# Optimization experiments

Measured on AMD Instinct MI355X. Metric: run time of the kernel, lower is better.

The kernel has to match this reference:

```python
import jax, jax.numpy as jnp
import numpy as np

V, T, H, N, HID = 512, 64, 256, 1024, 100
D = V + T  # biLSTM input dim


def _lstm_dir(x, Wih, Whh, b, reverse):
    # x: [n, Din]; PyTorch gate order i,f,g,o; b = b_ih + b_hh (equivalent math)
    xw = x @ Wih.T + b  # [n, 4H] precomputed input projection
    if reverse:
        xw = xw[::-1]
    h_dim = Whh.shape[1]

    def step(carry, xt):
        h, c = carry
        g = xt + h @ Whh.T
        i, f, gg, o = jnp.split(g, 4, axis=-1)
        i = jax.nn.sigmoid(i)
        f = jax.nn.sigmoid(f)
        gg = jnp.tanh(gg)
        o = jax.nn.sigmoid(o)
        c = f * c + i * gg
        h = o * jnp.tanh(c)
        return (h, c), h

    init = (jnp.zeros((h_dim,), x.dtype), jnp.zeros((h_dim,), x.dtype))
    _, hs = jax.lax.scan(step, init, xw)
    return hs[::-1] if reverse else hs


def setup_inputs() -> dict:
    key = jax.random.key(0)
    ks = jax.random.split(key, 20)
    s = 1.0 / np.sqrt(H)  # PyTorch LSTM init scale
    inp = {
        "word_table": jax.random.normal(ks[0], (V, V), jnp.float32) * 0.1,
        "pos_table": jax.random.normal(ks[1], (T, T), jnp.float32) * 0.1,
        # layer 0 fwd/bwd
        "l0f_Wih": jax.random.uniform(ks[2], (4 * H, D), jnp.float32, -s, s),
        "l0f_Whh": jax.random.uniform(ks[3], (4 * H, H), jnp.float32, -s, s),
        "l0f_b": jax.random.uniform(ks[4], (4 * H,), jnp.float32, -s, s),
        "l0b_Wih": jax.random.uniform(ks[5], (4 * H, D), jnp.float32, -s, s),
        "l0b_Whh": jax.random.uniform(ks[6], (4 * H, H), jnp.float32, -s, s),
        "l0b_b": jax.random.uniform(ks[7], (4 * H,), jnp.float32, -s, s),
        # layer 1 fwd/bwd (input = 2H)
        "l1f_Wih": jax.random.uniform(ks[8], (4 * H, 2 * H), jnp.float32, -s, s),
        "l1f_Whh": jax.random.uniform(ks[9], (4 * H, H), jnp.float32, -s, s),
        "l1f_b": jax.random.uniform(ks[10], (4 * H,), jnp.float32, -s, s),
        "l1b_Wih": jax.random.uniform(ks[11], (4 * H, 2 * H), jnp.float32, -s, s),
        "l1b_Whh": jax.random.uniform(ks[12], (4 * H, H), jnp.float32, -s, s),
        "l1b_b": jax.random.uniform(ks[13], (4 * H,), jnp.float32, -s, s),
        # edge-scorer MLP: Linear(4H,100) -> tanh -> Linear(100,1)
        "mlp_W1": jax.random.uniform(ks[14], (HID, 4 * H), jnp.float32, -0.03, 0.03),
        "mlp_b1": jax.random.uniform(ks[15], (HID,), jnp.float32, -0.03, 0.03),
        "mlp_W2": jax.random.uniform(ks[16], (1, HID), jnp.float32, -0.1, 0.1),
        "mlp_b2": jax.random.uniform(ks[17], (1,), jnp.float32, -0.1, 0.1),
        "word_idx": jax.random.randint(ks[18], (1, N), 0, V),
        "pos_idx": jax.random.randint(ks[19], (1, N), 0, T),
    }
    return inp


def reference(word_table, pos_table,
              l0f_Wih, l0f_Whh, l0f_b, l0b_Wih, l0b_Whh, l0b_b,
              l1f_Wih, l1f_Whh, l1f_b, l1b_Wih, l1b_Whh, l1b_b,
              mlp_W1, mlp_b1, mlp_W2, mlp_b2,
              word_idx, pos_idx):
    # embedding lookups on external tables, cat word+pos -> [n, D]
    x = jnp.concatenate([word_table[word_idx[0]], pos_table[pos_idx[0]]], axis=-1)
    # 2-layer bidirectional LSTM, batch=1 (squeezed)
    h = jnp.concatenate([_lstm_dir(x, l0f_Wih, l0f_Whh, l0f_b, False),
                         _lstm_dir(x, l0b_Wih, l0b_Whh, l0b_b, True)], axis=-1)  # [n, 2H]
    h = jnp.concatenate([_lstm_dir(h, l1f_Wih, l1f_Whh, l1f_b, False),
                         _lstm_dir(h, l1b_Wih, l1b_Whh, l1b_b, True)], axis=-1)  # [n, 2H]
    # pairwise edge scorer: layer_2(tanh(layer_1(cat(h_head, h_mod))))
    # split W1 = [Wh | Wm] so the cat never materializes per pair
    two_h = h.shape[-1]
    Wh, Wm = mlp_W1[:, :two_h], mlp_W1[:, two_h:]
    A = h @ Wh.T  # [n, HID] head contribution
    B = h @ Wm.T  # [n, HID] modifier contribution
    hid = jnp.tanh(A[:, None, :] + B[None, :, :] + mlp_b1)  # [n, n, HID]
    scores = hid @ mlp_W2[0] + mlp_b2[0]  # [n, n]
    n = scores.shape[0]
    eye = jnp.eye(n, dtype=bool)
    scores = jnp.where(eye, 0.0, scores)  # diagonal left at 0, as in the torch loop
    return jax.nn.softmax(scores, axis=0)
```

## Files before the change

kernel.cpp:

```cpp
#include <hip/hip_runtime.h>
#include <hip/hip_bf16.h>


#define L2E 1.4426950408889634f

__device__ __forceinline__ float fast_rcp(float x) { return __builtin_amdgcn_rcpf(x); }
__device__ __forceinline__ float sigm_f(float x) {
    return fast_rcp(1.f + exp2f(-x * L2E));
}
__device__ __forceinline__ float tanh_f(float x) {
    return 1.f - 2.f * fast_rcp(1.f + exp2f(x * (2.f * L2E)));
}

__device__ __forceinline__ void st_msg(unsigned long long* p, unsigned long long m) {
    asm volatile("global_store_dwordx2 %0, %1, off sc0 sc1"
                 :: "v"(p), "v"(m) : "memory");
}

__device__ __forceinline__ unsigned long long poll_msg(
    const unsigned long long* p, unsigned want)
{
    unsigned long long r0, r1, r2, r3, r = 0;
    bool done = false;
    for (int it = 0; it < 8192 && !done; ++it) {
        asm volatile(
            "global_load_dwordx2 %0, %4, off sc0 sc1\n\t"
            "global_load_dwordx2 %1, %4, off sc0 sc1\n\t"
            "global_load_dwordx2 %2, %4, off sc0 sc1\n\t"
            "global_load_dwordx2 %3, %4, off sc0 sc1\n\t"
            "s_waitcnt vmcnt(3)"
            : "=&v"(r0), "=&v"(r1), "=&v"(r2), "=&v"(r3)
            : "v"(p) : "memory");
        if (__all((unsigned)(r0 >> 32) == want)) { r = r0; done = true; }
        if (!done) {
            asm volatile("s_waitcnt vmcnt(2)" ::: "memory");
            if (__all((unsigned)(r1 >> 32) == want)) { r = r1; done = true; }
        }
        if (!done) {
            asm volatile("s_waitcnt vmcnt(1)" ::: "memory");
            if (__all((unsigned)(r2 >> 32) == want)) { r = r2; done = true; }
        }
        if (!done) {
            asm volatile("s_waitcnt vmcnt(0)" ::: "memory");
            if (__all((unsigned)(r3 >> 32) == want)) { r = r3; done = true; }
        }
        asm volatile("s_waitcnt vmcnt(0)" ::: "memory");
    }
    if (!done) {
        do {
            r = __hip_atomic_load(p, __ATOMIC_RELAXED, __HIP_MEMORY_SCOPE_AGENT);
        } while (!__all((unsigned)(r >> 32) == want));
    }
    return r;
}

__global__ __launch_bounds__(256) void embed_kernel(
    const float* __restrict__ wt, const float* __restrict__ pt,
    const int* __restrict__ wi, const int* __restrict__ pi,
    float* __restrict__ x)
{
    int idx = blockIdx.x * 256 + threadIdx.x;
    if (idx >= 1024 * 576) return;
    int n = idx / 576, c = idx % 576;
    x[idx] = (c < 512) ? wt[wi[n] * 512 + c] : pt[pi[n] * 64 + (c - 512)];
}

__global__ __launch_bounds__(256) void gemm_bias(
    const float* __restrict__ A,
    const float* __restrict__ W0, const float* __restrict__ W1,
    const float* __restrict__ b0, const float* __restrict__ b1,
    float* __restrict__ C0, float* __restrict__ C1,
    int M, int N, int K)
{
    const float* W = blockIdx.z ? W1 : W0;
    const float* bias = blockIdx.z ? b1 : b0;
    float* C = blockIdx.z ? C1 : C0;
    int m0 = blockIdx.y * 64, n0 = blockIdx.x * 64;
    __shared__ float As[16][65];
    __shared__ float Ws[16][65];
    int tid = threadIdx.x;
    int tx = tid & 15, ty = tid >> 4;
    float acc[4][4] = {};
    int lr = tid >> 2, lkc = (tid & 3) * 4;
    for (int k0 = 0; k0 < K; k0 += 16) {
        float4 a4 = *(const float4*)&A[(size_t)(m0 + lr) * K + k0 + lkc];
        float4 w4 = *(const float4*)&W[(size_t)(n0 + lr) * K + k0 + lkc];
        As[lkc + 0][lr] = a4.x; As[lkc + 1][lr] = a4.y;
        As[lkc + 2][lr] = a4.z; As[lkc + 3][lr] = a4.w;
        Ws[lkc + 0][lr] = w4.x; Ws[lkc + 1][lr] = w4.y;
        Ws[lkc + 2][lr] = w4.z; Ws[lkc + 3][lr] = w4.w;
        __syncthreads();
#pragma unroll
        for (int k = 0; k < 16; k++) {
            float a[4], b[4];
#pragma unroll
            for (int i = 0; i < 4; i++) a[i] = As[k][ty * 4 + i];
#pragma unroll
            for (int j = 0; j < 4; j++) b[j] = Ws[k][tx * 4 + j];
#pragma unroll
            for (int i = 0; i < 4; i++)
#pragma unroll
                for (int j = 0; j < 4; j++) acc[i][j] += a[i] * b[j];
        }
        __syncthreads();
    }
    int colbase = n0 + tx * 4;
    float4 bv = *(const float4*)&bias[colbase];
#pragma unroll
    for (int i = 0; i < 4; i++) {
        float4 o;
        o.x = acc[i][0] + bv.x; o.y = acc[i][1] + bv.y;
        o.z = acc[i][2] + bv.z; o.w = acc[i][3] + bv.w;
        *(float4*)&C[(size_t)(m0 + ty * 4 + i) * N + colbase] = o;
    }
}

__global__ __launch_bounds__(512, 2) void lstm_scan(
    const float* __restrict__ xw_f, const float* __restrict__ xw_b,
    const float* __restrict__ Whh_f, const float* __restrict__ Whh_b,
    float* __restrict__ hout,
    unsigned long long* __restrict__ hx)
{
    int slot = blockIdx.x & 7;
    int sub  = blockIdx.x >> 3;
    int dir;
    if (slot == 0) dir = 0;
    else if (slot == 4) dir = 1;
    else return;

    const float* __restrict__ xw  = dir ? xw_b : xw_f;
    const float* __restrict__ Whh = dir ? Whh_b : Whh_f;
    unsigned long long* __restrict__ hxd = hx + dir * 512;

    const int tid  = threadIdx.x;
    const int lane = tid & 63;
    const int wv   = tid >> 6;
    const int half = tid >> 8;
    const int lr   = tid & 255;
    const int gi   = lr >> 6;
    const int R    = gi * 256 + (sub << 6) + (lr & 63);

    float4 w4[32];
    {
        const float4* Wr = (const float4*)(Whh + (size_t)R * 256 + (half << 7));
#pragma unroll
        for (int i = 0; i < 32; i++) w4[i] = Wr[i];
    }

    __shared__ float h_sh[256];
    __shared__ float part[512];
    __shared__ float gact[256];

    float c = 0.f;
    float xwv = 0.f;
    if (tid < 256) xwv = xw[(size_t)(dir ? 1023 : 0) * 1024 + R];
    if (wv < 4) h_sh[(wv << 6) + lane] = 0.f;
    __syncthreads();

    for (int t = 0; t < 1024; t++) {
        float a0 = 0.f, a1 = 0.f, a2 = 0.f, a3 = 0.f;
        const float4* hp4 = (const float4*)&h_sh[half << 7];
#pragma unroll
        for (int i = 0; i < 32; i += 4) {
            float4 h0v = hp4[i + 0], w0v = w4[i + 0];
            float4 h1v = hp4[i + 1], w1v = w4[i + 1];
            float4 h2v = hp4[i + 2], w2v = w4[i + 2];
            float4 h3v = hp4[i + 3], w3v = w4[i + 3];
            a0 += w0v.x * h0v.x + w0v.y * h0v.y + w0v.z * h0v.z + w0v.w * h0v.w;
            a1 += w1v.x * h1v.x + w1v.y * h1v.y + w1v.z * h1v.z + w1v.w * h1v.w;
            a2 += w2v.x * h2v.x + w2v.y * h2v.y + w2v.z * h2v.z + w2v.w * h2v.w;
            a3 += w3v.x * h3v.x + w3v.y * h3v.y + w3v.z * h3v.z + w3v.w * h3v.w;
        }
        part[tid] = (a0 + a1) + (a2 + a3);
        __syncthreads();

        if (tid < 256) {
            float s = part[tid] + part[tid + 256] + xwv;
            gact[tid] = (gi == 2) ? tanh_f(s) : sigm_f(s);
            if (t + 1 < 1024) {
                int trown = dir ? (1022 - t) : (t + 1);
                xwv = xw[(size_t)trown * 1024 + R];
            }
        }
        __syncthreads();

        if (tid < 64) {
            float iv = gact[lane], fv = gact[64 + lane],
                  gv = gact[128 + lane], ov = gact[192 + lane];
            c = fv * c + iv * gv;
            float h = ov * tanh_f(c);
            if (t + 1 < 1024) {
                unsigned long long msg =
                    ((unsigned long long)(unsigned)(t + 1) << 32) |
                    (unsigned long long)__float_as_uint(h);
                st_msg(&hxd[(((sub << 1) + ((t + 1) & 1)) << 6) + lane], msg);
                h_sh[(sub << 6) + lane] = h;
            }
            int trow = dir ? (1023 - t) : t;
            hout[(size_t)trow * 512 + dir * 256 + (sub << 6) + lane] = h;
        } else if (wv <= 3 && t + 1 < 1024) {
            int pw = (sub + wv) & 3;
            const unsigned long long* sp =
                &hxd[(((pw << 1) + ((t + 1) & 1)) << 6) + lane];
            unsigned long long v = poll_msg(sp, (unsigned)(t + 1));
            h_sh[(pw << 6) + lane] = __uint_as_float((unsigned)v);
        }
        __syncthreads();

#pragma unroll
        for (int i = 0; i < 32; i++)
            asm volatile("" : "+v"(w4[i].x), "+v"(w4[i].y),
                              "+v"(w4[i].z), "+v"(w4[i].w));
    }
}

__global__ __launch_bounds__(256) void transpose_w1(
    const float* __restrict__ W1, float* __restrict__ W1T)
{
    int idx = blockIdx.x * 256 + threadIdx.x;
    if (idx >= 100 * 1024) return;
    int n = idx / 1024, j = idx % 1024;
    W1T[j * 100 + n] = W1[idx];
}

__global__ __launch_bounds__(256) void ab_kernel(
    const float* __restrict__ h1, const float* __restrict__ W1T,
    const float* __restrict__ b1v,
    float* __restrict__ Ab, float* __restrict__ Bb)
{
    int m0 = blockIdx.x * 16;
    __shared__ float hs[16][512];
    int tid = threadIdx.x;
    for (int idx = tid * 4; idx < 16 * 512; idx += 1024) {
        int r = idx >> 9, cc = idx & 511;
        *(float4*)&hs[r][cc] = *(const float4*)&h1[(size_t)(m0 + r) * 512 + cc];
    }
    __syncthreads();
    bool isB = tid >= 128;
    int n = tid & 127;
    if (n < 100) {
        float acc[16] = {};
        const float* wbase = W1T + (isB ? 512 * 100 : 0) + n;
#pragma unroll 4
        for (int k = 0; k < 512; k++) {
            float wv = wbase[k * 100];
#pragma unroll
            for (int m = 0; m < 16; m++) acc[m] += hs[m][k] * wv;
        }
        float badd = isB ? 0.f : b1v[n];
        float* dst = isB ? Bb : Ab;
#pragma unroll
        for (int m = 0; m < 16; m++) dst[(m0 + m) * 100 + n] = acc[m] + badd;
    }
}

__global__ __launch_bounds__(256) void pair_kernel(
    const float* __restrict__ Ab, const float* __restrict__ Bb,
    const float* __restrict__ W2, const float* __restrict__ b2,
    float* __restrict__ sT)
{
    int i0 = blockIdx.x * 32, j0 = blockIdx.y * 32;
    __shared__ float Ash[32][101];
    __shared__ float Bsh[32][101];
    __shared__ float w2s[100];
    int tid = threadIdx.x;
    for (int idx = tid; idx < 3200; idx += 256) {
        int r = idx / 100, cc = idx % 100;
        Ash[r][cc] = Ab[(i0 + r) * 100 + cc];
        Bsh[r][cc] = Bb[(j0 + r) * 100 + cc];
    }
    if (tid < 100) w2s[tid] = W2[tid];
    __syncthreads();
    float b2v = b2[0];
    int il = (tid & 15) * 2, jl = (tid >> 4) * 2;
    float a00 = 0.f, a01 = 0.f, a10 = 0.f, a11 = 0.f;
#pragma unroll 4
    for (int k = 0; k < 100; k++) {
        float wv = w2s[k];
        float x0 = Ash[il][k], x1 = Ash[il + 1][k];
        float y0 = Bsh[jl][k], y1 = Bsh[jl + 1][k];
        a00 += wv * tanh_f(x0 + y0);
        a01 += wv * tanh_f(x0 + y1);
        a10 += wv * tanh_f(x1 + y0);
        a11 += wv * tanh_f(x1 + y1);
    }
    float vals[2][2] = {{a00, a01}, {a10, a11}};
#pragma unroll
    for (int a = 0; a < 2; a++)
#pragma unroll
        for (int b = 0; b < 2; b++) {
            int gi2 = i0 + il + a, gj = j0 + jl + b;
            float v = vals[a][b] + b2v;
            if (gi2 == gj) v = 0.f;
            sT[(size_t)gj * 1024 + gi2] = v;
        }
}

__global__ __launch_bounds__(256) void colstats(
    const float* __restrict__ sT, float* __restrict__ mx, float* __restrict__ rs)
{
    int j = blockIdx.x;
    const float* row = sT + (size_t)j * 1024;
    int tid = threadIdx.x;
    __shared__ float red[256];
    float m = -INFINITY;
    for (int i = tid; i < 1024; i += 256) m = fmaxf(m, row[i]);
    red[tid] = m; __syncthreads();
    for (int s = 128; s > 0; s >>= 1) {
        if (tid < s) red[tid] = fmaxf(red[tid], red[tid + s]);
        __syncthreads();
    }
    float mxv = red[0];
    __syncthreads();
    float ssum = 0.f;
    for (int i = tid; i < 1024; i += 256) ssum += exp2f((row[i] - mxv) * L2E);
    red[tid] = ssum; __syncthreads();
    for (int s = 128; s > 0; s >>= 1) {
        if (tid < s) red[tid] += red[tid + s];
        __syncthreads();
    }
    if (tid == 0) { mx[j] = mxv; rs[j] = 1.f / red[0]; }
}

__global__ __launch_bounds__(256) void writeout(
    const float* __restrict__ sT, const float* __restrict__ mx,
    const float* __restrict__ rs, float* __restrict__ out)
{
    int i0 = blockIdx.x * 32, j0 = blockIdx.y * 32;
    __shared__ float til[32][33];
    int tid = threadIdx.x;
    int r = tid >> 3, c4 = (tid & 7) * 4;
    float4 v = *(const float4*)&sT[(size_t)(j0 + r) * 1024 + i0 + c4];
    til[r][c4 + 0] = v.x; til[r][c4 + 1] = v.y;
    til[r][c4 + 2] = v.z; til[r][c4 + 3] = v.w;
    __syncthreads();
    float4 o;
    float* op = &out[(size_t)(i0 + r) * 1024 + j0 + c4];
    o.x = exp2f((til[c4 + 0][r] - mx[j0 + c4 + 0]) * L2E) * rs[j0 + c4 + 0];
    o.y = exp2f((til[c4 + 1][r] - mx[j0 + c4 + 1]) * L2E) * rs[j0 + c4 + 1];
    o.z = exp2f((til[c4 + 2][r] - mx[j0 + c4 + 2]) * L2E) * rs[j0 + c4 + 2];
    o.w = exp2f((til[c4 + 3][r] - mx[j0 + c4 + 3]) * L2E) * rs[j0 + c4 + 3];
    *(float4*)op = o;
}

extern "C" void kernel_launch(void* const* d_in, const int* in_sizes, int n_in,
                              void* d_out, int out_size, void* d_ws, size_t ws_size,
                              hipStream_t stream)
{
    const float* word_table = (const float*)d_in[0];
    const float* pos_table  = (const float*)d_in[1];
    const float* l0f_Wih = (const float*)d_in[2];
    const float* l0f_Whh = (const float*)d_in[3];
    const float* l0f_b   = (const float*)d_in[4];
    const float* l0b_Wih = (const float*)d_in[5];
    const float* l0b_Whh = (const float*)d_in[6];
    const float* l0b_b   = (const float*)d_in[7];
    const float* l1f_Wih = (const float*)d_in[8];
    const float* l1f_Whh = (const float*)d_in[9];
    const float* l1f_b   = (const float*)d_in[10];
    const float* l1b_Wih = (const float*)d_in[11];
    const float* l1b_Whh = (const float*)d_in[12];
    const float* l1b_b   = (const float*)d_in[13];
    const float* mlp_W1  = (const float*)d_in[14];
    const float* mlp_b1  = (const float*)d_in[15];
    const float* mlp_W2  = (const float*)d_in[16];
    const float* mlp_b2  = (const float*)d_in[17];
    const int*   word_idx = (const int*)d_in[18];
    const int*   pos_idx  = (const int*)d_in[19];
    float* out = (float*)d_out;

    float* ws = (float*)d_ws;
    const size_t OFF_X   = 0;
    const size_t OFF_XWF = 589824;
    const size_t OFF_XWB = 1638400;
    const size_t OFF_H0  = 2686976;
    const size_t OFF_H1  = 3211264;
    const size_t OFF_W1T = 3735552;
    const size_t OFF_A   = 3837952;
    const size_t OFF_B   = 3940352;
    const size_t OFF_ST  = 4042752;
    const size_t OFF_MX  = 5091328;
    const size_t OFF_RS  = 5092352;
    const size_t OFF_HX  = 5095424;

    float* x   = ws + OFF_X;
    float* xwf = ws + OFF_XWF;
    float* xwb = ws + OFF_XWB;
    float* h0  = ws + OFF_H0;
    float* h1  = ws + OFF_H1;
    float* w1t = ws + OFF_W1T;
    float* Ab  = ws + OFF_A;
    float* Bb  = ws + OFF_B;
    float* sT  = ws + OFF_ST;
    float* mx  = ws + OFF_MX;
    float* rs  = ws + OFF_RS;
    unsigned long long* hx0 = (unsigned long long*)(ws + OFF_HX);
    unsigned long long* hx1 = hx0 + 1024;

    hipMemsetAsync(hx0, 0, 2048 * sizeof(unsigned long long), stream);

    embed_kernel<<<(1024 * 576 + 255) / 256, 256, 0, stream>>>(
        word_table, pos_table, word_idx, pos_idx, x);

    transpose_w1<<<(100 * 1024 + 255) / 256, 256, 0, stream>>>(mlp_W1, w1t);

    gemm_bias<<<dim3(16, 16, 2), 256, 0, stream>>>(
        x, l0f_Wih, l0b_Wih, l0f_b, l0b_b, xwf, xwb, 1024, 1024, 576);

    lstm_scan<<<32, 512, 0, stream>>>(
        xwf, xwb, l0f_Whh, l0b_Whh, h0, hx0);

    gemm_bias<<<dim3(16, 16, 2), 256, 0, stream>>>(
        h0, l1f_Wih, l1b_Wih, l1f_b, l1b_b, xwf, xwb, 1024, 1024, 512);

    lstm_scan<<<32, 512, 0, stream>>>(
        xwf, xwb, l1f_Whh, l1b_Whh, h1, hx1);

    ab_kernel<<<64, 256, 0, stream>>>(h1, w1t, mlp_b1, Ab, Bb);

    pair_kernel<<<dim3(32, 32), 256, 0, stream>>>(Ab, Bb, mlp_W2, mlp_b2, sT);

    colstats<<<1024, 256, 0, stream>>>(sT, mx, rs);

    writeout<<<dim3(32, 32), 256, 0, stream>>>(sT, mx, rs, out);
}
```

Before: 4.237 ms.

## Split LSTM recurrence across eight blocks each handling both directions

The recurrent scan now launches 8 blocks instead of 32 mostly-idle ones. Each block handles 32 hidden units of both the forward and the backward direction, with half its threads per direction. Each thread keeps 16 float4 weights in registers instead of 32, which halves the per-step matrix-vector work and register pressure per block. The cost is that every step now waits for h-exchange messages from 7 peers instead of 3, and those peers may sit on different XCDs, where they were previously grouped by block index. That can raise the per-step synchronization latency.

```diff
diff --git a/kernel.cpp b/kernel.cpp
--- a/kernel.cpp
+++ b/kernel.cpp
@@ -121,47 +121,45 @@
     float* __restrict__ hout,
     unsigned long long* __restrict__ hx)
 {
-    int slot = blockIdx.x & 7;
-    int sub  = blockIdx.x >> 3;
-    int dir;
-    if (slot == 0) dir = 0;
-    else if (slot == 4) dir = 1;
-    else return;
-
-    const float* __restrict__ xw  = dir ? xw_b : xw_f;
-    const float* __restrict__ Whh = dir ? Whh_b : Whh_f;
-    unsigned long long* __restrict__ hxd = hx + dir * 512;
-
+    const int sub  = blockIdx.x;
     const int tid  = threadIdx.x;
     const int lane = tid & 63;
     const int wv   = tid >> 6;
-    const int half = tid >> 8;
-    const int lr   = tid & 255;
-    const int gi   = lr >> 6;
-    const int R    = gi * 256 + (sub << 6) + (lr & 63);
-
-    float4 w4[32];
+    const int dsel = tid >> 8;
+    const int tl   = tid & 255;
+    const int kh   = tl >> 7;
+    const int lrow = tl & 127;
+    const int gi   = lrow >> 5;
+    const int R    = gi * 256 + sub * 32 + (lrow & 31);
+
+    const float* __restrict__ xw  = dsel ? xw_b : xw_f;
+    const float* __restrict__ Whh = dsel ? Whh_b : Whh_f;
+
+    float4 w4[16];
     {
-        const float4* Wr = (const float4*)(Whh + (size_t)R * 256 + (half << 7));
-#pragma unroll
-        for (int i = 0; i < 32; i++) w4[i] = Wr[i];
-    }
-
-    __shared__ float h_sh[256];
-    __shared__ float part[512];
-    __shared__ float gact[256];
+        const float4* Wr = (const float4*)(Whh + (size_t)R * 256 + (kh << 7));
+#pragma unroll
+        for (int i = 0; i < 16; i++) w4[i] = Wr[i];
+    }
+
+    __shared__ float h0_sh[256], h1_sh[256];
+    __shared__ float part0[256], part1[256];
+    __shared__ float gact0[128], gact1[128];
+    float* __restrict__ h_sh  = dsel ? h1_sh : h0_sh;
+    float* __restrict__ partd = dsel ? part1 : part0;
+    float* __restrict__ gactd = dsel ? gact1 : gact0;
 
     float c = 0.f;
     float xwv = 0.f;
-    if (tid < 256) xwv = xw[(size_t)(dir ? 1023 : 0) * 1024 + R];
-    if (wv < 4) h_sh[(wv << 6) + lane] = 0.f;
+    if (tl < 128) xwv = xw[(size_t)(dsel ? 1023 : 0) * 1024 + R];
+    if (tid < 256) { h0_sh[tid] = 0.f; h1_sh[tid] = 0.f; }
     __syncthreads();
 
     for (int t = 0; t < 1024; t++) {
         float a0 = 0.f, a1 = 0.f, a2 = 0.f, a3 = 0.f;
-        const float4* hp4 = (const float4*)&h_sh[half << 7];
-#pragma unroll
-        for (int i = 0; i < 32; i += 4) {
+        const float4* hp4 = (const float4*)&h_sh[kh << 7];
+#pragma unroll
+        for (int i = 0; i < 16; i += 4) {
             float4 h0v = hp4[i + 0], w0v = w4[i + 0];
             float4 h1v = hp4[i + 1], w1v = w4[i + 1];
             float4 h2v = hp4[i + 2], w2v = w4[i + 2];
@@ -171,44 +169,49 @@
             a2 += w2v.x * h2v.x + w2v.y * h2v.y + w2v.z * h2v.z + w2v.w * h2v.w;
             a3 += w3v.x * h3v.x + w3v.y * h3v.y + w3v.z * h3v.z + w3v.w * h3v.w;
         }
-        part[tid] = (a0 + a1) + (a2 + a3);
-        __syncthreads();
-
-        if (tid < 256) {
-            float s = part[tid] + part[tid + 256] + xwv;
-            gact[tid] = (gi == 2) ? tanh_f(s) : sigm_f(s);
+        partd[tl] = (a0 + a1) + (a2 + a3);
+        __syncthreads();
+
+        if (tl < 128) {
+            float s = partd[tl] + partd[128 + tl] + xwv;
+            gactd[tl] = (gi == 2) ? tanh_f(s) : sigm_f(s);
             if (t + 1 < 1024) {
-                int trown = dir ? (1022 - t) : (t + 1);
+                int trown = dsel ? (1022 - t) : (t + 1);
                 xwv = xw[(size_t)trown * 1024 + R];
             }
         }
         __syncthreads();
 
-        if (tid < 64) {
-            float iv = gact[lane], fv = gact[64 + lane],
-                  gv = gact[128 + lane], ov = gact[192 + lane];
-            c = fv * c + iv * gv;
-            float h = ov * tanh_f(c);
-            if (t + 1 < 1024) {
-                unsigned long long msg =
-                    ((unsigned long long)(unsigned)(t + 1) << 32) |
-                    (unsigned long long)__float_as_uint(h);
-                st_msg(&hxd[(((sub << 1) + ((t + 1) & 1)) << 6) + lane], msg);
-                h_sh[(sub << 6) + lane] = h;
+        const int par = (t + 1) & 1;
+        if (wv == 0 || wv == 4) {
+            if (lane < 32) {
+                float iv = gactd[lane], fv = gactd[32 + lane],
+                      gv = gactd[64 + lane], ov = gactd[96 + lane];
+                c = fv * c + iv * gv;
+                float h = ov * tanh_f(c);
+                if (t + 1 < 1024) {
+                    unsigned long long msg =
+                        ((unsigned long long)(unsigned)(t + 1) << 32) |
+                        (unsigned long long)__float_as_uint(h);
+                    st_msg(&hx[(((sub << 1) + par) << 6) + (dsel << 5) + lane], msg);
+                    h_sh[sub * 32 + lane] = h;
+                }
+                int trow = dsel ? (1023 - t) : t;
+                hout[(size_t)trow * 512 + (dsel << 8) + sub * 32 + lane] = h;
             }
-            int trow = dir ? (1023 - t) : t;
-            hout[(size_t)trow * 512 + dir * 256 + (sub << 6) + lane] = h;
-        } else if (wv <= 3 && t + 1 < 1024) {
-            int pw = (sub + wv) & 3;
+        }
+        if (wv != 0 && t + 1 < 1024) {
+            int pw = (sub + wv) & 7;
             const unsigned long long* sp =
-                &hxd[(((pw << 1) + ((t + 1) & 1)) << 6) + lane];
+                &hx[(((pw << 1) + par) << 6) + lane];
             unsigned long long v = poll_msg(sp, (unsigned)(t + 1));
-            h_sh[(pw << 6) + lane] = __uint_as_float((unsigned)v);
-        }
-        __syncthreads();
-
-#pragma unroll
-        for (int i = 0; i < 32; i++)
+            float hv = __uint_as_float((unsigned)v);
+            ((lane < 32) ? h0_sh : h1_sh)[pw * 32 + (lane & 31)] = hv;
+        }
+        __syncthreads();
+
+#pragma unroll
+        for (int i = 0; i < 16; i++)
             asm volatile("" : "+v"(w4[i].x), "+v"(w4[i].y),
                               "+v"(w4[i].z), "+v"(w4[i].w));
     }
@@ -407,13 +410,13 @@
     gemm_bias<<<dim3(16, 16, 2), 256, 0, stream>>>(
         x, l0f_Wih, l0b_Wih, l0f_b, l0b_b, xwf, xwb, 1024, 1024, 576);
 
-    lstm_scan<<<32, 512, 0, stream>>>(
+    lstm_scan<<<8, 512, 0, stream>>>(
         xwf, xwb, l0f_Whh, l0b_Whh, h0, hx0);
 
     gemm_bias<<<dim3(16, 16, 2), 256, 0, stream>>>(
         h0, l1f_Wih, l1b_Wih, l1f_b, l1b_b, xwf, xwb, 1024, 1024, 512);
 
-    lstm_scan<<<32, 512, 0, stream>>>(
+    lstm_scan<<<8, 512, 0, stream>>>(
         xwf, xwb, l1f_Whh, l1b_Whh, h1, hx1);
 
     ab_kernel<<<64, 256, 0, stream>>>(h1, w1t, mlp_b1, Ab, Bb);
```

Measured after the change: 4.087 ms. 1.04x faster.
